# Kernel tuning notes

Measured on AMD Instinct MI355X. Metric: run time of the kernel, lower is better.

## Reference

```python
import jax, jax.numpy as jnp
import numpy as np

B, N, DIM, HEADS, FFN, H, W = 8, 100, 256, 8, 2048, 128, 128
M = H * W
HD = DIM // HEADS
EPS = 1e-5


def ln(x, g, b):
    mu = jnp.mean(x, axis=-1, keepdims=True)
    var = jnp.mean(jnp.square(x - mu), axis=-1, keepdims=True)
    return (x - mu) * jax.lax.rsqrt(var + EPS) * g + b


def setup_inputs() -> dict:
    key = jax.random.key(0)
    ks = jax.random.split(key, 20)
    w = lambda k, shape: jax.random.normal(k, shape, jnp.float32) * 0.02
    inp = {
        "x": jax.random.normal(ks[0], (B, N, DIM), jnp.float32),
        "context": jax.random.normal(ks[1], (B, M, DIM), jnp.float32),
        "mask": jax.random.randint(ks[2], (B, N, H, W), 0, 2, jnp.int32),
        # masked cross-attention params
        "mq_w": w(ks[3], (DIM, DIM)), "mq_b": jnp.zeros((DIM,), jnp.float32),
        "mkv_w": w(ks[4], (2 * DIM, DIM)), "mkv_b": jnp.zeros((2 * DIM,), jnp.float32),
        "mproj_w": w(ks[5], (DIM, DIM)), "mproj_b": jnp.zeros((DIM,), jnp.float32),
        # nn.MultiheadAttention params
        "in_w": w(ks[6], (3 * DIM, DIM)), "in_b": jnp.zeros((3 * DIM,), jnp.float32),
        "out_w": w(ks[7], (DIM, DIM)), "out_b": jnp.zeros((DIM,), jnp.float32),
        # FFN params
        "w1": w(ks[8], (FFN, DIM)), "b1": jnp.zeros((FFN,), jnp.float32),
        "w2": w(ks[9], (DIM, FFN)), "b2": jnp.zeros((DIM,), jnp.float32),
        # LayerNorm params
        "n1_g": jnp.ones((DIM,), jnp.float32), "n1_b": jnp.zeros((DIM,), jnp.float32),
        "n2_g": jnp.ones((DIM,), jnp.float32), "n2_b": jnp.zeros((DIM,), jnp.float32),
        "n3_g": jnp.ones((DIM,), jnp.float32), "n3_b": jnp.zeros((DIM,), jnp.float32),
        "n4_g": jnp.ones((DIM,), jnp.float32), "n4_b": jnp.zeros((DIM,), jnp.float32),
    }
    return inp


def reference(x, context, mask, mq_w, mq_b, mkv_w, mkv_b, mproj_w, mproj_b,
              in_w, in_b, out_w, out_b, w1, b1, w2, b2,
              n1_g, n1_b, n2_g, n2_b, n3_g, n3_b, n4_g, n4_b):
    b, n, _ = x.shape
    m = context.shape[1]
    scale = HD ** -0.5

    # ---- masked cross-attention (pre-norm1, residual) ----
    res = x
    y = ln(x, n1_g, n1_b)
    q = (y @ mq_w.T + mq_b).reshape(b, n, HEADS, HD).transpose(0, 2, 1, 3)        # [b,h,n,d]
    kv = (context @ mkv_w.T + mkv_b).reshape(b, m, 2, HEADS, HD)
    k = kv[:, :, 0].transpose(0, 2, 1, 3)                                         # [b,h,m,d]
    v = kv[:, :, 1].transpose(0, 2, 1, 3)
    dots = jnp.einsum('bhnd,bhmd->bhnm', q, k) * scale                            # [b,h,n,m]
    mflat = mask.reshape(b, n, m)[:, None]                                        # [b,1,n,m]
    dots = jnp.where(mflat == 0, -jnp.inf, dots)
    attn = jax.nn.softmax(dots, axis=-1)
    o = jnp.einsum('bhnm,bhmd->bhnd', attn, v).transpose(0, 2, 1, 3).reshape(b, n, DIM)
    x = res + (o @ mproj_w.T + mproj_b)

    # ---- self-attention: torch MHA without batch_first, so seq axis = b, batch axis = n ----
    res = x
    y = ln(x, n2_g, n2_b)
    qkv = y @ in_w.T + in_b                                                       # [b,n,3*dim]
    sq, sk, sv = jnp.split(qkv, 3, axis=-1)
    sq = sq.reshape(b, n, HEADS, HD) * scale
    sk = sk.reshape(b, n, HEADS, HD)
    sv = sv.reshape(b, n, HEADS, HD)
    satt = jax.nn.softmax(jnp.einsum('inhd,jnhd->nhij', sq, sk), axis=-1)         # attn over seq=b
    so = jnp.einsum('nhij,jnhd->inhd', satt, sv).reshape(b, n, DIM)
    x = res + (so @ out_w.T + out_b)

    # ---- FFN ----
    res = x
    y = ln(x, n3_g, n3_b)
    f = jax.nn.gelu(y @ w1.T + b1, approximate=False) @ w2.T + b2
    x = res + f

    return ln(x, n4_g, n4_b)
```

## Files before the change

### kernel.cpp

```cpp
#include <hip/hip_runtime.h>
#include <hip/hip_bf16.h>

#define BB 8
#define NN 100
#define DIMM 256
#define HEADSS 8
#define HDD 32
#define FFNN 2048
#define MM 16384
#define ROWS (BB*NN)
#define CTX_ROWS (BB*MM)
#define SCALE 0.17677669529663689f

typedef __attribute__((ext_vector_type(8))) short s16x8;
typedef __attribute__((ext_vector_type(4))) float f32x4;

__device__ inline ushort f2bf(float f) {
    union { float f; unsigned u; } c; c.f = f;
    unsigned r = c.u + 0x7fffu + ((c.u >> 16) & 1u);
    return (ushort)(r >> 16);
}
__device__ inline float bf2f(ushort u) {
    union { unsigned i; float f; } c; c.i = ((unsigned)u) << 16; return c.f;
}

__global__ __launch_bounds__(256) void conv_bf16(const float* __restrict__ src,
                                                 ushort* __restrict__ dst, int n4) {
    int i = blockIdx.x * 256 + threadIdx.x;
    if (i < n4) {
        float4 v = ((const float4*)src)[i];
        union { ushort u[4]; uint2 v2; } o;
        o.u[0] = f2bf(v.x); o.u[1] = f2bf(v.y); o.u[2] = f2bf(v.z); o.u[3] = f2bf(v.w);
        *(uint2*)&dst[i * 4] = o.v2;
    }
}

__global__ void ln_kernel(const float* __restrict__ x, const float* __restrict__ g,
                          const float* __restrict__ beta, float* __restrict__ y) {
    int row = blockIdx.x;
    int t = threadIdx.x;
    float v = x[row * 256 + t];
    __shared__ float red[256];
    red[t] = v; __syncthreads();
    for (int s = 128; s > 0; s >>= 1) { if (t < s) red[t] += red[t + s]; __syncthreads(); }
    float mu = red[0] * (1.0f / 256.0f);
    __syncthreads();
    float d = v - mu;
    red[t] = d * d; __syncthreads();
    for (int s = 128; s > 0; s >>= 1) { if (t < s) red[t] += red[t + s]; __syncthreads(); }
    float var = red[0] * (1.0f / 256.0f);
    float r = rsqrtf(var + 1e-5f);
    y[row * 256 + t] = d * r * g[t] + beta[t];
}

template<bool GELU, bool RES>
__global__ __launch_bounds__(256) void gemm_proj(const float* __restrict__ A,
                                                 const float* __restrict__ W,
                                                 const float* __restrict__ bias,
                                                 const float* __restrict__ res,
                                                 float* __restrict__ out,
                                                 int M, int K, int C) {
    int bm = blockIdx.x, bn = blockIdx.y;
    __shared__ __align__(16) ushort As[64 * 64];
    __shared__ __align__(16) ushort Bs[64 * 64];
    int t = threadIdx.x;
    int lane = t & 63, w = t >> 6;
    int wr = w >> 1, wc = w & 1;
    int l15 = lane & 15, lk = lane >> 4;
    int l7 = l15 & 7;

    f32x4 acc[2][2];
    #pragma unroll
    for (int i = 0; i < 2; i++)
        #pragma unroll
        for (int j = 0; j < 2; j++)
            acc[i][j] = (f32x4){0.f, 0.f, 0.f, 0.f};

    int srow = t >> 2;
    int sg0 = (t & 3) * 2;
    int swz0 = (sg0 ^ (srow & 7)) * 8;
    int swz1 = ((sg0 + 1) ^ (srow & 7)) * 8;
    int scol = sg0 * 8;

    int nkt = K >> 6;
    for (int kt = 0; kt < nkt; ++kt) {
        int kb = kt * 64 + scol;
        {
            int gr = bm * 64 + srow;
            s16x8 va0 = {0,0,0,0,0,0,0,0}, va1 = {0,0,0,0,0,0,0,0};
            if (gr < M) {
                const float* ap = A + (size_t)gr * K + kb;
                float4 a0 = *(const float4*)ap;
                float4 a1 = *(const float4*)(ap + 4);
                float4 a2 = *(const float4*)(ap + 8);
                float4 a3 = *(const float4*)(ap + 12);
                va0[0] = (short)f2bf(a0.x); va0[1] = (short)f2bf(a0.y);
                va0[2] = (short)f2bf(a0.z); va0[3] = (short)f2bf(a0.w);
                va0[4] = (short)f2bf(a1.x); va0[5] = (short)f2bf(a1.y);
                va0[6] = (short)f2bf(a1.z); va0[7] = (short)f2bf(a1.w);
                va1[0] = (short)f2bf(a2.x); va1[1] = (short)f2bf(a2.y);
                va1[2] = (short)f2bf(a2.z); va1[3] = (short)f2bf(a2.w);
                va1[4] = (short)f2bf(a3.x); va1[5] = (short)f2bf(a3.y);
                va1[6] = (short)f2bf(a3.z); va1[7] = (short)f2bf(a3.w);
            }
            *(s16x8*)&As[srow * 64 + swz0] = va0;
            *(s16x8*)&As[srow * 64 + swz1] = va1;
            const float* bp = W + (size_t)(bn * 64 + srow) * K + kb;
            float4 b0 = *(const float4*)bp;
            float4 b1 = *(const float4*)(bp + 4);
            float4 b2 = *(const float4*)(bp + 8);
            float4 b3 = *(const float4*)(bp + 12);
            s16x8 vb0, vb1;
            vb0[0] = (short)f2bf(b0.x); vb0[1] = (short)f2bf(b0.y);
            vb0[2] = (short)f2bf(b0.z); vb0[3] = (short)f2bf(b0.w);
            vb0[4] = (short)f2bf(b1.x); vb0[5] = (short)f2bf(b1.y);
            vb0[6] = (short)f2bf(b1.z); vb0[7] = (short)f2bf(b1.w);
            vb1[0] = (short)f2bf(b2.x); vb1[1] = (short)f2bf(b2.y);
            vb1[2] = (short)f2bf(b2.z); vb1[3] = (short)f2bf(b2.w);
            vb1[4] = (short)f2bf(b3.x); vb1[5] = (short)f2bf(b3.y);
            vb1[6] = (short)f2bf(b3.z); vb1[7] = (short)f2bf(b3.w);
            *(s16x8*)&Bs[srow * 64 + swz0] = vb0;
            *(s16x8*)&Bs[srow * 64 + swz1] = vb1;
        }
        __syncthreads();
        #pragma unroll
        for (int kk = 0; kk < 64; kk += 32) {
            int gsw = (((kk >> 3) + lk) ^ l7) * 8;
            s16x8 af[2], bf[2];
            #pragma unroll
            for (int mi = 0; mi < 2; mi++)
                af[mi] = *(const s16x8*)&As[(wr * 32 + mi * 16 + l15) * 64 + gsw];
            #pragma unroll
            for (int ni = 0; ni < 2; ni++)
                bf[ni] = *(const s16x8*)&Bs[(wc * 32 + ni * 16 + l15) * 64 + gsw];
            #pragma unroll
            for (int mi = 0; mi < 2; mi++)
                #pragma unroll
                for (int ni = 0; ni < 2; ni++)
                    acc[mi][ni] = __builtin_amdgcn_mfma_f32_16x16x32_bf16(af[mi], bf[ni], acc[mi][ni], 0, 0, 0);
        }
        __syncthreads();
    }
    #pragma unroll
    for (int ni = 0; ni < 2; ni++) {
        int col = bn * 64 + wc * 32 + ni * 16 + l15;
        float bv = bias[col];
        #pragma unroll
        for (int mi = 0; mi < 2; mi++) {
            int row0 = bm * 64 + wr * 32 + mi * 16 + lk * 4;
            #pragma unroll
            for (int r = 0; r < 4; r++) {
                int gr = row0 + r;
                if (gr < M) {
                    float v = acc[mi][ni][r] + bv;
                    if (GELU) v = 0.5f * v * (1.0f + erff(v * 0.70710678118654752f));
                    if (RES)  v += res[(size_t)gr * C + col];
                    out[(size_t)gr * C + col] = v;
                }
            }
        }
    }
}

__global__ __launch_bounds__(256) void gemm_kv(const float* __restrict__ A,
                                               const ushort* __restrict__ Wbf,
                                               const float* __restrict__ bias,
                                               ushort* __restrict__ Kh,
                                               ushort* __restrict__ Vh) {
    int i = blockIdx.x;
    int bm = ((i >> 5) << 3) + (i & 7);
    int bn = (i >> 3) & 3;
    __shared__ __align__(16) ushort As[128 * 64];
    __shared__ __align__(16) ushort Bs[128 * 64];
    int t = threadIdx.x;
    int lane = t & 63;
    int w = t >> 6;
    int wr = w >> 1, wc = w & 1;
    int l15 = lane & 15, lk = lane >> 4;
    int l7 = l15 & 7;

    f32x4 acc[4][4];
    #pragma unroll
    for (int ii = 0; ii < 4; ii++)
        #pragma unroll
        for (int j = 0; j < 4; j++)
            acc[ii][j] = (f32x4){0.f, 0.f, 0.f, 0.f};

    int srow = t >> 3;
    int sg   = t & 7;
    int skk  = sg * 8;
    int swz  = (sg ^ (srow & 7)) * 8;

    const float*  Abase = A   + (size_t)(bm * 128) * 256;
    const ushort* Bbase = Wbf + (size_t)(bn * 128) * 256;

    float4 ra[4][2];
    uint4  rb[4];

    {
        int kbase = 0;
        #pragma unroll
        for (int p = 0; p < 4; p++) {
            int row = p * 32 + srow;
            const float* ap = Abase + (size_t)row * 256 + kbase + skk;
            ra[p][0] = *(const float4*)ap;
            ra[p][1] = *(const float4*)(ap + 4);
            rb[p] = *(const uint4*)(Bbase + (size_t)row * 256 + kbase + skk);
        }
    }

    for (int kt = 0; kt < 4; ++kt) {
        #pragma unroll
        for (int p = 0; p < 4; p++) {
            int row = p * 32 + srow;
            s16x8 va;
            va[0] = (short)f2bf(ra[p][0].x); va[1] = (short)f2bf(ra[p][0].y);
            va[2] = (short)f2bf(ra[p][0].z); va[3] = (short)f2bf(ra[p][0].w);
            va[4] = (short)f2bf(ra[p][1].x); va[5] = (short)f2bf(ra[p][1].y);
            va[6] = (short)f2bf(ra[p][1].z); va[7] = (short)f2bf(ra[p][1].w);
            *(s16x8*)&As[row * 64 + swz] = va;
            *(uint4*)&Bs[row * 64 + swz] = rb[p];
        }
        __syncthreads();
        if (kt < 3) {
            int kbase = (kt + 1) * 64;
            #pragma unroll
            for (int p = 0; p < 4; p++) {
                int row = p * 32 + srow;
                const float* ap = Abase + (size_t)row * 256 + kbase + skk;
                ra[p][0] = *(const float4*)ap;
                ra[p][1] = *(const float4*)(ap + 4);
                rb[p] = *(const uint4*)(Bbase + (size_t)row * 256 + kbase + skk);
            }
        }
        #pragma unroll
        for (int kk = 0; kk < 64; kk += 32) {
            int gsw = (((kk >> 3) + lk) ^ l7) * 8;
            s16x8 af[4], bf[4];
            #pragma unroll
            for (int mi = 0; mi < 4; mi++)
                af[mi] = *(const s16x8*)&As[(wr * 64 + mi * 16 + l15) * 64 + gsw];
            #pragma unroll
            for (int ni = 0; ni < 4; ni++)
                bf[ni] = *(const s16x8*)&Bs[(wc * 64 + ni * 16 + l15) * 64 + gsw];
            #pragma unroll
            for (int mi = 0; mi < 4; mi++)
                #pragma unroll
                for (int ni = 0; ni < 4; ni++)
                    acc[mi][ni] = __builtin_amdgcn_mfma_f32_16x16x32_bf16(af[mi], bf[ni], acc[mi][ni], 0, 0, 0);
        }
        __syncthreads();
    }
    #pragma unroll
    for (int ni = 0; ni < 4; ni++) {
        int col = bn * 128 + wc * 64 + ni * 16 + l15;
        float bv = bias[col];
        int isV = col >> 8;
        int c2 = col & 255;
        int h = c2 >> 5, hd = c2 & 31;
        ushort* dst = isV ? Vh : Kh;
        #pragma unroll
        for (int mi = 0; mi < 4; mi++) {
            int row0 = bm * 128 + wr * 64 + mi * 16 + lk * 4;
            #pragma unroll
            for (int r = 0; r < 4; r++) {
                int gr = row0 + r;
                int b = gr >> 14, m = gr & 16383;
                dst[(((size_t)(b * 8 + h)) * 16384 + m) * 32 + hd] = f2bf(acc[mi][ni][r] + bv);
            }
        }
    }
}

__global__ __launch_bounds__(256) void pack_mask(const int* __restrict__ mask,
                                                 unsigned* __restrict__ Mb) {
    unsigned tid = blockIdx.x * 256 + threadIdx.x;
    int b = tid >> 21;
    int rem = tid & ((1u << 21) - 1);
    int n = rem >> 14;
    int m = rem & 16383;
    int mv = 0;
    if (n < 100) mv = mask[(((size_t)b * 100 + n) << 14) + m];
    unsigned long long bal = __ballot(mv != 0);
    if ((threadIdx.x & 63) == 0) {
        size_t widx = (((size_t)b * 128 + n) << 9) + (m >> 5);
        *(unsigned long long*)(Mb + widx) = bal;
    }
}

__global__ __launch_bounds__(256) void xattn_flash(
        const float* __restrict__ q,
        const ushort* __restrict__ Kh,
        const ushort* __restrict__ Vh,
        const unsigned* __restrict__ Mb,
        float* __restrict__ O_part,
        float* __restrict__ m_part,
        float* __restrict__ l_part) {
    int ch = blockIdx.x;
    int h = blockIdx.y, b = blockIdx.z;
    int t = threadIdx.x;
    int lane = t & 63, w = t >> 6;
    int l15 = lane & 15, g = lane >> 4;

    __shared__ __align__(16) ushort Qs[128 * 40];
    __shared__ __align__(16) ushort Ks[64 * 40];
    __shared__ __align__(16) ushort Vt[32 * 72];
    __shared__ __align__(16) ushort Ps[128 * 72];
    __shared__ unsigned Ms[128 * 64];

    {
        int r = t >> 1, dh = (t & 1) * 16;
        s16x8 v0 = {0,0,0,0,0,0,0,0}, v1 = {0,0,0,0,0,0,0,0};
        if (r < 100) {
            const float* qp = q + ((size_t)(b * 100 + r)) * 256 + h * 32 + dh;
            #pragma unroll
            for (int j = 0; j < 8; j++) v0[j] = (short)f2bf(qp[j] * SCALE);
            #pragma unroll
            for (int j = 0; j < 8; j++) v1[j] = (short)f2bf(qp[8 + j] * SCALE);
        }
        *(s16x8*)&Qs[r * 40 + dh] = v0;
        *(s16x8*)&Qs[r * 40 + dh + 8] = v1;
    }
    {
        const unsigned* mp = Mb + (((size_t)b * 128) << 9) + ch * 64;
        #pragma unroll
        for (int i = 0; i < 32; i++) {
            int idx = t + i * 256;
            int r = idx >> 6, wd = idx & 63;
            Ms[idx] = mp[((size_t)r << 9) + wd];
        }
    }
    __syncthreads();

    s16x8 aq[2];
    aq[0] = *(const s16x8*)&Qs[(w * 32 + l15) * 40 + g * 8];
    aq[1] = *(const s16x8*)&Qs[(w * 32 + 16 + l15) * 40 + g * 8];

    float m_run[2][4], l_run[2][4];
    f32x4 accO[2][2];
    #pragma unroll
    for (int qt = 0; qt < 2; qt++) {
        #pragma unroll
        for (int r = 0; r < 4; r++) { m_run[qt][r] = -1e30f; l_run[qt][r] = 0.f; }
        accO[qt][0] = (f32x4){0.f,0.f,0.f,0.f};
        accO[qt][1] = (f32x4){0.f,0.f,0.f,0.f};
    }

    const ushort* Kbase = Kh + (((size_t)(b * 8 + h)) * 16384 + (size_t)ch * 2048) * 32;
    const ushort* Vbase = Vh + (((size_t)(b * 8 + h)) * 16384 + (size_t)ch * 2048) * 32;

    for (int tile = 0; tile < 32; ++tile) {
        if (tile) __syncthreads();
        {
            int mrow = t >> 2, d0 = (t & 3) * 8;
            uint4 k4 = *(const uint4*)(Kbase + ((size_t)(tile * 64 + mrow)) * 32 + d0);
            *(uint4*)&Ks[mrow * 40 + d0] = k4;
            uint4 v4 = *(const uint4*)(Vbase + ((size_t)(tile * 64 + mrow)) * 32 + d0);
            const ushort* vsp = (const ushort*)&v4;
            #pragma unroll
            for (int j = 0; j < 8; j++) Vt[(d0 + j) * 72 + mrow] = vsp[j];
        }
        __syncthreads();

        s16x8 bk[4];
        #pragma unroll
        for (int ni = 0; ni < 4; ni++)
            bk[ni] = *(const s16x8*)&Ks[(ni * 16 + l15) * 40 + g * 8];
        f32x4 sfrag[2][4];
        #pragma unroll
        for (int qt = 0; qt < 2; qt++)
            #pragma unroll
            for (int ni = 0; ni < 4; ni++)
                sfrag[qt][ni] = __builtin_amdgcn_mfma_f32_16x16x32_bf16(
                    aq[qt], bk[ni], (f32x4){0.f,0.f,0.f,0.f}, 0, 0, 0);

        #pragma unroll
        for (int qt = 0; qt < 2; qt++) {
            #pragma unroll
            for (int r = 0; r < 4; r++) {
                int qrow = w * 32 + qt * 16 + g * 4 + r;
                unsigned wd0 = Ms[qrow * 64 + tile * 2];
                unsigned wd1 = Ms[qrow * 64 + tile * 2 + 1];
                float sv[4];
                float mx = -1e30f;
                #pragma unroll
                for (int ni = 0; ni < 4; ni++) {
                    unsigned wdx = (ni < 2) ? wd0 : wd1;
                    unsigned bit = (wdx >> ((ni & 1) * 16 + l15)) & 1u;
                    sv[ni] = bit ? sfrag[qt][ni][r] : -1e30f;
                    mx = fmaxf(mx, sv[ni]);
                }
                mx = fmaxf(mx, __shfl_xor(mx, 1));
                mx = fmaxf(mx, __shfl_xor(mx, 2));
                mx = fmaxf(mx, __shfl_xor(mx, 4));
                mx = fmaxf(mx, __shfl_xor(mx, 8));
                float mnew = fmaxf(m_run[qt][r], mx);
                float corr = __expf(m_run[qt][r] - mnew);
                m_run[qt][r] = mnew;
                float rowsum = 0.f;
                #pragma unroll
                for (int ni = 0; ni < 4; ni++) {
                    float pv = __expf(sv[ni] - mnew);
                    rowsum += pv;
                    Ps[qrow * 72 + ni * 16 + l15] = f2bf(pv);
                }
                rowsum += __shfl_xor(rowsum, 1);
                rowsum += __shfl_xor(rowsum, 2);
                rowsum += __shfl_xor(rowsum, 4);
                rowsum += __shfl_xor(rowsum, 8);
                l_run[qt][r] = l_run[qt][r] * corr + rowsum;
                accO[qt][0][r] *= corr;
                accO[qt][1][r] *= corr;
            }
        }

        s16x8 ap0[2], ap1[2], bv0[2], bv1[2];
        #pragma unroll
        for (int qt = 0; qt < 2; qt++) {
            ap0[qt] = *(const s16x8*)&Ps[(w * 32 + qt * 16 + l15) * 72 + g * 8];
            ap1[qt] = *(const s16x8*)&Ps[(w * 32 + qt * 16 + l15) * 72 + 32 + g * 8];
        }
        #pragma unroll
        for (int dt = 0; dt < 2; dt++) {
            bv0[dt] = *(const s16x8*)&Vt[(dt * 16 + l15) * 72 + g * 8];
            bv1[dt] = *(const s16x8*)&Vt[(dt * 16 + l15) * 72 + 32 + g * 8];
        }
        #pragma unroll
        for (int qt = 0; qt < 2; qt++)
            #pragma unroll
            for (int dt = 0; dt < 2; dt++) {
                accO[qt][dt] = __builtin_amdgcn_mfma_f32_16x16x32_bf16(ap0[qt], bv0[dt], accO[qt][dt], 0, 0, 0);
                accO[qt][dt] = __builtin_amdgcn_mfma_f32_16x16x32_bf16(ap1[qt], bv1[dt], accO[qt][dt], 0, 0, 0);
            }
    }

    size_t pbase = ((size_t)(b * 8 + h) * 8 + ch) * 128;
    #pragma unroll
    for (int qt = 0; qt < 2; qt++) {
        #pragma unroll
        for (int r = 0; r < 4; r++) {
            int qrow = w * 32 + qt * 16 + g * 4 + r;
            #pragma unroll
            for (int dt = 0; dt < 2; dt++)
                O_part[(pbase + qrow) * 32 + dt * 16 + l15] = accO[qt][dt][r];
            if (l15 == 0) {
                m_part[pbase + qrow] = m_run[qt][r];
                l_part[pbase + qrow] = l_run[qt][r];
            }
        }
    }
}

__global__ __launch_bounds__(256) void xattn_combine(
        const float* __restrict__ O_part, const float* __restrict__ m_part,
        const float* __restrict__ l_part, float* __restrict__ o) {
    int n = blockIdx.x;
    int b = blockIdx.y;
    int t = threadIdx.x;
    int h = t >> 5, d = t & 31;
    size_t base = ((size_t)(b * 8 + h)) * 8;
    float gm = -1e30f;
    #pragma unroll
    for (int ch = 0; ch < 8; ch++)
        gm = fmaxf(gm, m_part[(base + ch) * 128 + n]);
    float L = 0.f, acc = 0.f;
    #pragma unroll
    for (int ch = 0; ch < 8; ch++) {
        float e = __expf(m_part[(base + ch) * 128 + n] - gm);
        L += l_part[(base + ch) * 128 + n] * e;
        acc += O_part[((base + ch) * 128 + n) * 32 + d] * e;
    }
    o[((size_t)(b * 100 + n)) * 256 + t] = acc / L;
}

__global__ void sattn_kernel(const float* __restrict__ qkv, float* __restrict__ so) {
    int n = blockIdx.x;
    int t = threadIdx.x;
    __shared__ float sq[8][256], sk[8][256], sv[8][256];
    __shared__ float S[512];
    for (int idx = t; idx < 8 * 768; idx += 256) {
        int i = idx / 768, c = idx - i * 768;
        float v = qkv[((size_t)(i * NN + n)) * 768 + c];
        if (c < 256) sq[i][c] = v * SCALE;
        else if (c < 512) sk[i][c - 256] = v;
        else sv[i][c - 512] = v;
    }
    __syncthreads();
    for (int idx = t; idx < 512; idx += 256) {
        int h = idx >> 6, i = (idx >> 3) & 7, j = idx & 7;
        float acc = 0.0f;
        #pragma unroll
        for (int d = 0; d < 32; d++) acc += sq[i][h * 32 + d] * sk[j][h * 32 + d];
        S[idx] = acc;
    }
    __syncthreads();
    if (t < 64) {
        int h = t >> 3, i = t & 7;
        float* row = &S[h * 64 + i * 8];
        float mx = row[0];
        #pragma unroll
        for (int j = 1; j < 8; j++) mx = fmaxf(mx, row[j]);
        float sum = 0.0f;
        #pragma unroll
        for (int j = 0; j < 8; j++) { row[j] = __expf(row[j] - mx); sum += row[j]; }
        float inv = 1.0f / sum;
        #pragma unroll
        for (int j = 0; j < 8; j++) row[j] *= inv;
    }
    __syncthreads();
    int c = t, h = t >> 5;
    #pragma unroll
    for (int i = 0; i < 8; i++) {
        float acc = 0.0f;
        #pragma unroll
        for (int j = 0; j < 8; j++) acc += S[h * 64 + i * 8 + j] * sv[j][c];
        so[((size_t)(i * NN + n)) * 256 + c] = acc;
    }
}

extern "C" void kernel_launch(void* const* d_in, const int* in_sizes, int n_in,
                              void* d_out, int out_size, void* d_ws, size_t ws_size,
                              hipStream_t stream) {
    const float* x      = (const float*)d_in[0];
    const float* ctx    = (const float*)d_in[1];
    const int*   mask   = (const int*)  d_in[2];
    const float* mq_w   = (const float*)d_in[3];
    const float* mq_b   = (const float*)d_in[4];
    const float* mkv_w  = (const float*)d_in[5];
    const float* mkv_b  = (const float*)d_in[6];
    const float* mproj_w= (const float*)d_in[7];
    const float* mproj_b= (const float*)d_in[8];
    const float* in_w   = (const float*)d_in[9];
    const float* in_b   = (const float*)d_in[10];
    const float* out_w  = (const float*)d_in[11];
    const float* out_b  = (const float*)d_in[12];
    const float* w1     = (const float*)d_in[13];
    const float* b1     = (const float*)d_in[14];
    const float* w2     = (const float*)d_in[15];
    const float* b2     = (const float*)d_in[16];
    const float* n1_g   = (const float*)d_in[17];
    const float* n1_b   = (const float*)d_in[18];
    const float* n2_g   = (const float*)d_in[19];
    const float* n2_b   = (const float*)d_in[20];
    const float* n3_g   = (const float*)d_in[21];
    const float* n3_b   = (const float*)d_in[22];
    const float* n4_g   = (const float*)d_in[23];
    const float* n4_b   = (const float*)d_in[24];

    float* ws = (float*)d_ws;
    float* Y1  = ws + 0;
    float* Q   = ws + 204800;
    float* O   = ws + 409600;
    float* X1  = ws + 614400;
    float* Y2  = ws + 819200;
    float* QKV = ws + 1024000;
    float* SO  = ws + 1638400;
    float* X2  = ws + 1843200;
    float* Y3  = ws + 2048000;
    float* F1  = ws + 2252800;
    float* X3  = ws + 3891200;
    unsigned* Mb     = (unsigned*)(ws + 819200);
    float*    O_part = ws + 1343488;
    float*    m_part = ws + 3440640;
    float*    l_part = ws + 3506176;
    ushort*   Wkv_bf = (ushort*)(ws + 3571712);
    ushort* Kh = (ushort*)((char*)d_ws + 16384000);
    ushort* Vh = (ushort*)((char*)d_ws + 16384000 + 67108864);

    float* out = (float*)d_out;

    ln_kernel<<<ROWS, 256, 0, stream>>>(x, n1_g, n1_b, Y1);
    gemm_proj<false, false><<<dim3(13, 4), 256, 0, stream>>>(
        Y1, mq_w, mq_b, nullptr, Q, ROWS, 256, 256);
    conv_bf16<<<128, 256, 0, stream>>>(mkv_w, Wkv_bf, 32768);
    gemm_kv<<<4096, 256, 0, stream>>>(ctx, Wkv_bf, mkv_b, Kh, Vh);
    pack_mask<<<(BB * 128 * MM) / 256, 256, 0, stream>>>(mask, Mb);
    {
        dim3 grid(8, HEADSS, BB);
        xattn_flash<<<grid, 256, 0, stream>>>(Q, Kh, Vh, Mb, O_part, m_part, l_part);
        dim3 cgrid(NN, BB);
        xattn_combine<<<cgrid, 256, 0, stream>>>(O_part, m_part, l_part, O);
    }
    gemm_proj<false, true><<<dim3(13, 4), 256, 0, stream>>>(
        O, mproj_w, mproj_b, x, X1, ROWS, 256, 256);
    ln_kernel<<<ROWS, 256, 0, stream>>>(X1, n2_g, n2_b, Y2);
    gemm_proj<false, false><<<dim3(13, 12), 256, 0, stream>>>(
        Y2, in_w, in_b, nullptr, QKV, ROWS, 256, 768);
    sattn_kernel<<<NN, 256, 0, stream>>>(QKV, SO);
    gemm_proj<false, true><<<dim3(13, 4), 256, 0, stream>>>(
        SO, out_w, out_b, X1, X2, ROWS, 256, 256);
    ln_kernel<<<ROWS, 256, 0, stream>>>(X2, n3_g, n3_b, Y3);
    gemm_proj<true, false><<<dim3(13, 32), 256, 0, stream>>>(
        Y3, w1, b1, nullptr, F1, ROWS, 256, FFNN);
    gemm_proj<false, true><<<dim3(13, 4), 256, 0, stream>>>(
        F1, w2, b2, X2, X3, ROWS, FFNN, 256);
    ln_kernel<<<ROWS, 256, 0, stream>>>(X3, n4_g, n4_b, out);
}
```

Before: 647.1 us.

## Compute full 512-wide KV output per block to read and convert context once

The context K/V projection now uses one 512-thread block per 128 context rows and covers all 512 output columns (K and V), instead of four blocks each covering 128 columns. The fp32 context tile is loaded and converted to bf16 only once rather than four times, which cuts global reads of the large context tensor. The cost is a larger LDS footprint (80KB), more accumulator registers per thread (128 floats) and fewer blocks, so occupancy may drop.

```diff
diff --git a/kernel.cpp b/kernel.cpp
--- a/kernel.cpp
+++ b/kernel.cpp
@@ -162,111 +162,114 @@
     }
 }
 
-__global__ __launch_bounds__(256) void gemm_kv(const float* __restrict__ A,
-                                               const ushort* __restrict__ Wbf,
-                                               const float* __restrict__ bias,
-                                               ushort* __restrict__ Kh,
-                                               ushort* __restrict__ Vh) {
-    int i = blockIdx.x;
-    int bm = ((i >> 5) << 3) + (i & 7);
-    int bn = (i >> 3) & 3;
+__global__ __launch_bounds__(512) void gemm_kv2(const float* __restrict__ A,
+                                                const ushort* __restrict__ Wbf,
+                                                const float* __restrict__ bias,
+                                                ushort* __restrict__ Kh,
+                                                ushort* __restrict__ Vh) {
+    int bm = blockIdx.x;
     __shared__ __align__(16) ushort As[128 * 64];
-    __shared__ __align__(16) ushort Bs[128 * 64];
+    __shared__ __align__(16) ushort Bs[512 * 64];
     int t = threadIdx.x;
-    int lane = t & 63;
-    int w = t >> 6;
-    int wr = w >> 1, wc = w & 1;
+    int lane = t & 63, w = t >> 6;
+    int wr = w >> 2, wc = w & 3;
     int l15 = lane & 15, lk = lane >> 4;
     int l7 = l15 & 7;
 
-    f32x4 acc[4][4];
-    #pragma unroll
-    for (int ii = 0; ii < 4; ii++)
-        #pragma unroll
-        for (int j = 0; j < 4; j++)
-            acc[ii][j] = (f32x4){0.f, 0.f, 0.f, 0.f};
-
-    int srow = t >> 3;
-    int sg   = t & 7;
-    int skk  = sg * 8;
-    int swz  = (sg ^ (srow & 7)) * 8;
-
-    const float*  Abase = A   + (size_t)(bm * 128) * 256;
-    const ushort* Bbase = Wbf + (size_t)(bn * 128) * 256;
-
-    float4 ra[4][2];
-    uint4  rb[4];
+    f32x4 acc[4][8];
+    #pragma unroll
+    for (int i = 0; i < 4; i++)
+        #pragma unroll
+        for (int j = 0; j < 8; j++)
+            acc[i][j] = (f32x4){0.f, 0.f, 0.f, 0.f};
+
+    int arow = t >> 2;
+    int aq = t & 3;
+    int aswz0 = ((aq * 2)     ^ (arow & 7)) * 8;
+    int aswz1 = ((aq * 2 + 1) ^ (arow & 7)) * 8;
+    int brow = t >> 3;
+    int bsg = t & 7;
+    int bswz = (bsg ^ (brow & 7)) * 8;
+
+    const float* Ab = A + (size_t)(bm * 128) * 256;
+
+    float4 ra[4];
+    uint4  rb[8];
 
     {
-        int kbase = 0;
-        #pragma unroll
-        for (int p = 0; p < 4; p++) {
-            int row = p * 32 + srow;
-            const float* ap = Abase + (size_t)row * 256 + kbase + skk;
-            ra[p][0] = *(const float4*)ap;
-            ra[p][1] = *(const float4*)(ap + 4);
-            rb[p] = *(const uint4*)(Bbase + (size_t)row * 256 + kbase + skk);
-        }
+        const float* ap = Ab + (size_t)arow * 256 + aq * 16;
+        ra[0] = *(const float4*)ap;       ra[1] = *(const float4*)(ap + 4);
+        ra[2] = *(const float4*)(ap + 8); ra[3] = *(const float4*)(ap + 12);
+        #pragma unroll
+        for (int p = 0; p < 8; p++)
+            rb[p] = *(const uint4*)(Wbf + (size_t)(p * 64 + brow) * 256 + bsg * 8);
     }
 
     for (int kt = 0; kt < 4; ++kt) {
-        #pragma unroll
-        for (int p = 0; p < 4; p++) {
-            int row = p * 32 + srow;
-            s16x8 va;
-            va[0] = (short)f2bf(ra[p][0].x); va[1] = (short)f2bf(ra[p][0].y);
-            va[2] = (short)f2bf(ra[p][0].z); va[3] = (short)f2bf(ra[p][0].w);
-            va[4] = (short)f2bf(ra[p][1].x); va[5] = (short)f2bf(ra[p][1].y);
-            va[6] = (short)f2bf(ra[p][1].z); va[7] = (short)f2bf(ra[p][1].w);
-            *(s16x8*)&As[row * 64 + swz] = va;
-            *(uint4*)&Bs[row * 64 + swz] = rb[p];
+        {
+            s16x8 va0, va1;
+            va0[0] = (short)f2bf(ra[0].x); va0[1] = (short)f2bf(ra[0].y);
+            va0[2] = (short)f2bf(ra[0].z); va0[3] = (short)f2bf(ra[0].w);
+            va0[4] = (short)f2bf(ra[1].x); va0[5] = (short)f2bf(ra[1].y);
+            va0[6] = (short)f2bf(ra[1].z); va0[7] = (short)f2bf(ra[1].w);
+            va1[0] = (short)f2bf(ra[2].x); va1[1] = (short)f2bf(ra[2].y);
+            va1[2] = (short)f2bf(ra[2].z); va1[3] = (short)f2bf(ra[2].w);
+            va1[4] = (short)f2bf(ra[3].x); va1[5] = (short)f2bf(ra[3].y);
+            va1[6] = (short)f2bf(ra[3].z); va1[7] = (short)f2bf(ra[3].w);
+            *(s16x8*)&As[arow * 64 + aswz0] = va0;
+            *(s16x8*)&As[arow * 64 + aswz1] = va1;
+            #pragma unroll
+            for (int p = 0; p < 8; p++)
+                *(uint4*)&Bs[(p * 64 + brow) * 64 + bswz] = rb[p];
+        }
+        if (kt < 3) {
+            int kb = (kt + 1) * 64;
+            const float* ap = Ab + (size_t)arow * 256 + kb + aq * 16;
+            ra[0] = *(const float4*)ap;       ra[1] = *(const float4*)(ap + 4);
+            ra[2] = *(const float4*)(ap + 8); ra[3] = *(const float4*)(ap + 12);
+            #pragma unroll
+            for (int p = 0; p < 8; p++)
+                rb[p] = *(const uint4*)(Wbf + (size_t)(p * 64 + brow) * 256 + kb + bsg * 8);
         }
         __syncthreads();
-        if (kt < 3) {
-            int kbase = (kt + 1) * 64;
-            #pragma unroll
-            for (int p = 0; p < 4; p++) {
-                int row = p * 32 + srow;
-                const float* ap = Abase + (size_t)row * 256 + kbase + skk;
-                ra[p][0] = *(const float4*)ap;
-                ra[p][1] = *(const float4*)(ap + 4);
-                rb[p] = *(const uint4*)(Bbase + (size_t)row * 256 + kbase + skk);
-            }
-        }
         #pragma unroll
         for (int kk = 0; kk < 64; kk += 32) {
             int gsw = (((kk >> 3) + lk) ^ l7) * 8;
-            s16x8 af[4], bf[4];
+            s16x8 af[4], bf8[8];
             #pragma unroll
             for (int mi = 0; mi < 4; mi++)
                 af[mi] = *(const s16x8*)&As[(wr * 64 + mi * 16 + l15) * 64 + gsw];
             #pragma unroll
-            for (int ni = 0; ni < 4; ni++)
-                bf[ni] = *(const s16x8*)&Bs[(wc * 64 + ni * 16 + l15) * 64 + gsw];
+            for (int ni = 0; ni < 8; ni++)
+                bf8[ni] = *(const s16x8*)&Bs[(wc * 128 + ni * 16 + l15) * 64 + gsw];
             #pragma unroll
             for (int mi = 0; mi < 4; mi++)
                 #pragma unroll
-                for (int ni = 0; ni < 4; ni++)
-                    acc[mi][ni] = __builtin_amdgcn_mfma_f32_16x16x32_bf16(af[mi], bf[ni], acc[mi][ni], 0, 0, 0);
+                for (int ni = 0; ni < 8; ni++)
+                    acc[mi][ni] = __builtin_amdgcn_mfma_f32_16x16x32_bf16(af[mi], bf8[ni], acc[mi][ni], 0, 0, 0);
         }
         __syncthreads();
     }
-    #pragma unroll
-    for (int ni = 0; ni < 4; ni++) {
-        int col = bn * 128 + wc * 64 + ni * 16 + l15;
-        float bv = bias[col];
-        int isV = col >> 8;
-        int c2 = col & 255;
-        int h = c2 >> 5, hd = c2 & 31;
-        ushort* dst = isV ? Vh : Kh;
-        #pragma unroll
-        for (int mi = 0; mi < 4; mi++) {
-            int row0 = bm * 128 + wr * 64 + mi * 16 + lk * 4;
-            #pragma unroll
-            for (int r = 0; r < 4; r++) {
-                int gr = row0 + r;
-                int b = gr >> 14, m = gr & 16383;
-                dst[(((size_t)(b * 8 + h)) * 16384 + m) * 32 + hd] = f2bf(acc[mi][ni][r] + bv);
+
+    float bv[8];
+    #pragma unroll
+    for (int ni = 0; ni < 8; ni++)
+        bv[ni] = bias[wc * 128 + ni * 16 + l15];
+    #pragma unroll
+    for (int mi = 0; mi < 4; mi++) {
+        #pragma unroll
+        for (int r = 0; r < 4; r++) {
+            int gr = bm * 128 + wr * 64 + mi * 16 + lk * 4 + r;
+            int b = gr >> 14, m = gr & 16383;
+            size_t base = ((size_t)(b * 8) * 16384 + m) * 32;
+            #pragma unroll
+            for (int ni = 0; ni < 8; ni++) {
+                int col = wc * 128 + ni * 16 + l15;
+                int isV = col >> 8;
+                int c2 = col & 255;
+                int h = c2 >> 5, hd = c2 & 31;
+                ushort* dst = isV ? Vh : Kh;
+                dst[base + (size_t)h * 16384 * 32 + hd] = f2bf(acc[mi][ni][r] + bv[ni]);
             }
         }
     }
@@ -573,7 +576,7 @@
     gemm_proj<false, false><<<dim3(13, 4), 256, 0, stream>>>(
         Y1, mq_w, mq_b, nullptr, Q, ROWS, 256, 256);
     conv_bf16<<<128, 256, 0, stream>>>(mkv_w, Wkv_bf, 32768);
-    gemm_kv<<<4096, 256, 0, stream>>>(ctx, Wkv_bf, mkv_b, Kh, Vh);
+    gemm_kv2<<<1024, 512, 0, stream>>>(ctx, Wkv_bf, mkv_b, Kh, Vh);
     pack_mask<<<(BB * 128 * MM) / 256, 256, 0, stream>>>(mask, Mb);
     {
         dim3 grid(8, HEADSS, BB);
```

After: 629.9 us. 1.03x faster.
